# Kernel optimization log

Measured on AMD Instinct MI355X. Metric: run time of the kernel, lower is better.

Reference implementation:

```python
import jax, jax.numpy as jnp
import numpy as np

BATCH, FEAT, N_IN, N_OUT = 2, 16, 2048, 4096  # nodes=N_IN, hyperedges=N_OUT
AVG_INCIDENCE = 3.0  # avg nodes per hyperedge


def setup_inputs() -> dict:
    key = jax.random.key(0)
    kx, kb = jax.random.split(key)
    x = jax.random.normal(kx, (BATCH, FEAT, N_IN), dtype=jnp.float32)
    # Bt = incidenceMatrix.T, shape [n_out_nodes, n_in_nodes], binary {0,1}
    Bt = (jax.random.uniform(kb, (N_OUT, N_IN)) < (AVG_INCIDENCE / N_IN)).astype(jnp.float32)
    return {"x": x, "Bt": Bt}


def reference(x, Bt):
    # Faithful to PoolCliqueToLine.forward:
    #   v[b, c, m] = max_n x[b, c, n] * Bt[m, n]
    # The torch code loops over batch and 8-feature chunks doing the same dense
    # broadcast-multiply + max; here it is fully vectorized in one expression.
    # Note: because Bt is mostly zero, the dense max implicitly clamps at 0
    # (x * 0 terms participate in the max), exactly as in the original.
    # intermediate: [B, C, M, N]
    return jnp.max(x[:, :, None, :] * Bt[None, None, :, :], axis=-1)
```

## Files before the change

kernel.cpp:

```cpp
#include <hip/hip_runtime.h>


#define HG_N_IN   2048
#define HG_N_OUT  4096
#define HG_BC     32
#define HG_RPB    16

__global__ __launch_bounds__(1024) void hg_rowmax(const float4* __restrict__ Bt4,
                                                  const float* __restrict__ x,
                                                  float* __restrict__ out) {
    __shared__ float r[HG_RPB][HG_BC + 1];
    const int w    = threadIdx.x >> 6;
    const int lane = threadIdx.x & 63;
    const int m0   = blockIdx.x * HG_RPB;
    const int m    = m0 + w;

    const float4* row = Bt4 + (size_t)m * (HG_N_IN / 4);
    float4 v[8];
    #pragma unroll
    for (int i = 0; i < 8; ++i) v[i] = row[lane + (i << 6)];

    const float* xr = x + (size_t)(lane & (HG_BC - 1)) * HG_N_IN;
    float mx = -INFINITY;
    int cnt = 0;

    #pragma unroll
    for (int i = 0; i < 8; ++i) {
        int code = (v[i].x != 0.0f) | ((v[i].y != 0.0f) << 1) |
                   ((v[i].z != 0.0f) << 2) | ((v[i].w != 0.0f) << 3);
        unsigned long long b = __ballot(code != 0);
        if (b == 0ull) continue;
        while (b) {
            int s = __ffsll((unsigned long long)b) - 1;
            b &= b - 1;
            int c = __shfl(code, s);
            int nbase = (s + (i << 6)) << 2;
            while (c) {
                int j = __ffs(c) - 1;
                c &= c - 1;
                ++cnt;
                if (lane < HG_BC) mx = fmaxf(mx, xr[nbase + j]);
            }
        }
    }

    float res = (cnt == HG_N_IN) ? mx : fmaxf(mx, 0.0f);
    if (lane < HG_BC) r[w][lane] = res;
    __syncthreads();

    const int t = threadIdx.x;
    if (t < HG_BC * HG_RPB) {
        const int bc = t >> 4;
        const int dm = t & (HG_RPB - 1);
        out[(size_t)bc * HG_N_OUT + m0 + dm] = r[dm][bc];
    }
}

extern "C" void kernel_launch(void* const* d_in, const int* in_sizes, int n_in,
                              void* d_out, int out_size, void* d_ws, size_t ws_size,
                              hipStream_t stream) {
    const float* x    = (const float*)d_in[0];
    const float4* Bt4 = (const float4*)d_in[1];
    float* out = (float*)d_out;

    hg_rowmax<<<HG_N_OUT / HG_RPB, 1024, 0, stream>>>(Bt4, x, out);
}
```

Measured before the change: 12.32 us.

## Use nontemporal Bt loads, per-component ballots, and smaller row blocks

Streams the 32MB incidence matrix with nontemporal loads so it does not pollute the cache that holds x. It replaces the shuffle-and-decode loop over nonzero lanes with four per-component ballots, which removes the shfl and the nested bit loop. Blocks now cover 8 rows with 512 threads instead of 16 rows with 1024, doubling the grid for finer scheduling. Extra ballots add a little work on chunks that contain nonzeros.

```diff
diff --git a/kernel.cpp b/kernel.cpp
--- a/kernel.cpp
+++ b/kernel.cpp
@@ -4,21 +4,24 @@
 #define HG_N_IN   2048
 #define HG_N_OUT  4096
 #define HG_BC     32
-#define HG_RPB    16
+#define HG_RPB    8
 
-__global__ __launch_bounds__(1024) void hg_rowmax(const float4* __restrict__ Bt4,
-                                                  const float* __restrict__ x,
-                                                  float* __restrict__ out) {
+typedef float nf4 __attribute__((ext_vector_type(4)));
+
+__global__ __launch_bounds__(512) void hg_rowmax(const nf4* __restrict__ Bt4,
+                                                 const float* __restrict__ x,
+                                                 float* __restrict__ out) {
     __shared__ float r[HG_RPB][HG_BC + 1];
     const int w    = threadIdx.x >> 6;
     const int lane = threadIdx.x & 63;
     const int m0   = blockIdx.x * HG_RPB;
     const int m    = m0 + w;
 
-    const float4* row = Bt4 + (size_t)m * (HG_N_IN / 4);
-    float4 v[8];
+    const nf4* row = Bt4 + (size_t)m * (HG_N_IN / 4);
+    nf4 v[8];
     #pragma unroll
-    for (int i = 0; i < 8; ++i) v[i] = row[lane + (i << 6)];
+    for (int i = 0; i < 8; ++i)
+        v[i] = __builtin_nontemporal_load(&row[lane + (i << 6)]);
 
     const float* xr = x + (size_t)(lane & (HG_BC - 1)) * HG_N_IN;
     float mx = -INFINITY;
@@ -26,20 +29,22 @@
 
     #pragma unroll
     for (int i = 0; i < 8; ++i) {
-        int code = (v[i].x != 0.0f) | ((v[i].y != 0.0f) << 1) |
-                   ((v[i].z != 0.0f) << 2) | ((v[i].w != 0.0f) << 3);
-        unsigned long long b = __ballot(code != 0);
-        if (b == 0ull) continue;
-        while (b) {
-            int s = __ffsll((unsigned long long)b) - 1;
-            b &= b - 1;
-            int c = __shfl(code, s);
-            int nbase = (s + (i << 6)) << 2;
-            while (c) {
-                int j = __ffs(c) - 1;
-                c &= c - 1;
+        const int f0 = (v[i].x != 0.0f), f1 = (v[i].y != 0.0f);
+        const int f2 = (v[i].z != 0.0f), f3 = (v[i].w != 0.0f);
+        unsigned long long any = __ballot((f0 | f1 | f2 | f3) != 0);
+        if (any == 0ull) continue;
+        unsigned long long bm[4];
+        bm[0] = __ballot(f0); bm[1] = __ballot(f1);
+        bm[2] = __ballot(f2); bm[3] = __ballot(f3);
+        #pragma unroll
+        for (int j = 0; j < 4; ++j) {
+            unsigned long long b = bm[j];
+            while (b) {
+                int s = __ffsll(b) - 1;
+                b &= b - 1;
                 ++cnt;
-                if (lane < HG_BC) mx = fmaxf(mx, xr[nbase + j]);
+                int n = (((i << 6) + s) << 2) + j;
+                if (lane < HG_BC) mx = fmaxf(mx, xr[n]);
             }
         }
     }
@@ -50,7 +55,7 @@
 
     const int t = threadIdx.x;
     if (t < HG_BC * HG_RPB) {
-        const int bc = t >> 4;
+        const int bc = t >> 3;
         const int dm = t & (HG_RPB - 1);
         out[(size_t)bc * HG_N_OUT + m0 + dm] = r[dm][bc];
     }
@@ -59,9 +64,9 @@
 extern "C" void kernel_launch(void* const* d_in, const int* in_sizes, int n_in,
                               void* d_out, int out_size, void* d_ws, size_t ws_size,
                               hipStream_t stream) {
-    const float* x    = (const float*)d_in[0];
-    const float4* Bt4 = (const float4*)d_in[1];
+    const float* x  = (const float*)d_in[0];
+    const nf4* Bt4  = (const nf4*)d_in[1];
     float* out = (float*)d_out;
 
-    hg_rowmax<<<HG_N_OUT / HG_RPB, 1024, 0, stream>>>(Bt4, x, out);
+    hg_rowmax<<<HG_N_OUT / HG_RPB, 512, 0, stream>>>(Bt4, x, out);
 }
```

Measured after the change: 11.59 us. -5.9%, faster.
